# Kernel optimization log

Measured on AMD Instinct MI355X. Metric: run time of the kernel, lower is better.

The kernel has to match this reference:

```python
import jax, jax.numpy as jnp
import numpy as np

V, E, HID, T, B, S = 50000, 256, 512, 9, 64, 512
H = HID // 2
START, STOP = T - 2, T - 1
NEG = -100000.0


def setup_inputs() -> dict:
    key = jax.random.key(0)
    ks = jax.random.split(key, 16)
    sc = 0.05
    tr = jax.random.normal(ks[15], (T, T), jnp.float32)
    tr = tr.at[STOP, :].set(NEG).at[:, START].set(NEG)
    return {
        "batchSentence": jax.random.randint(ks[0], (B, S), 0, V),
        "batchTag": jax.random.randint(ks[1], (B, S), 0, T - 2),
        "lenList": jax.random.randint(ks[2], (B,), 1, S + 1),
        "emb": jax.random.normal(ks[3], (V, E), jnp.float32) * sc,
        "w_ih0": jax.random.normal(ks[4], (2, 4 * H, E), jnp.float32) * sc,
        "w_hh0": jax.random.normal(ks[5], (2, 4 * H, H), jnp.float32) * sc,
        "b_ih0": jax.random.normal(ks[6], (2, 4 * H), jnp.float32) * sc,
        "b_hh0": jax.random.normal(ks[7], (2, 4 * H), jnp.float32) * sc,
        "w_ih1": jax.random.normal(ks[8], (2, 4 * H, 2 * H), jnp.float32) * sc,
        "w_hh1": jax.random.normal(ks[9], (2, 4 * H, H), jnp.float32) * sc,
        "b_ih1": jax.random.normal(ks[10], (2, 4 * H), jnp.float32) * sc,
        "b_hh1": jax.random.normal(ks[11], (2, 4 * H), jnp.float32) * sc,
        "fc_w": jax.random.normal(ks[12], (T, HID), jnp.float32) * sc,
        "fc_b": jax.random.normal(ks[13], (T,), jnp.float32) * sc,
        "transitions": tr,
    }


def _lstm_dir(xs, w_ih, w_hh, b_ih, b_hh, reverse):
    # xs: [S, B, in]; PyTorch gate order i, f, g, o
    h0 = jnp.zeros((xs.shape[1], w_hh.shape[1]), xs.dtype)
    b = b_ih + b_hh

    def step(carry, x_t):
        h, c = carry
        g = x_t @ w_ih.T + h @ w_hh.T + b
        i, f, gg, o = jnp.split(g, 4, axis=-1)
        c = jax.nn.sigmoid(f) * c + jax.nn.sigmoid(i) * jnp.tanh(gg)
        h = jax.nn.sigmoid(o) * jnp.tanh(c)
        return (h, c), h

    _, hs = jax.lax.scan(step, (h0, h0), xs, reverse=reverse)
    return hs


def _bilstm(x, layers):
    xs = x.transpose(1, 0, 2)  # [S, B, E]
    for w_ih, w_hh, b_ih, b_hh in layers:
        fwd = _lstm_dir(xs, w_ih[0], w_hh[0], b_ih[0], b_hh[0], False)
        bwd = _lstm_dir(xs, w_ih[1], w_hh[1], b_ih[1], b_hh[1], True)
        xs = jnp.concatenate([fwd, bwd], axis=-1)
    return xs.transpose(1, 0, 2)  # [B, S, 2H]


def _crf_forward(feats, mask, trans):
    # feats: [B, S, T], mask: [B, S] (t < length)
    start = jnp.full((feats.shape[0], feats.shape[2]), NEG, feats.dtype).at[:, START].set(0.0)

    def step(alpha, inp):
        ft, mt = inp  # [B, T], [B]
        new = jax.nn.logsumexp(alpha[:, :, None] + trans[None, :, :], axis=1) + ft
        return jnp.where(mt[:, None], new, alpha), None

    alpha, _ = jax.lax.scan(step, start, (feats.transpose(1, 0, 2), mask.T))
    return jax.nn.logsumexp(alpha + trans[None, :, STOP], axis=1)


def _gold_score(feats, tags, lengths, trans):
    # Faithful to original _score_sentence, incl. the feats[i][tags[i+1]] indexing
    Ss = feats.shape[1]
    pos = jnp.arange(Ss)
    pair_valid = (pos[None, :-1] + 1) < lengths[:, None]  # step i -> i+1 exists
    em0 = jnp.take_along_axis(feats[:, 0, :], tags[:, :1], axis=1)[:, 0]
    em_shift = jnp.take_along_axis(feats[:, :-1, :], tags[:, 1:, None], axis=2)[:, :, 0]
    tr = trans[tags[:, :-1], tags[:, 1:]]
    body = jnp.sum(jnp.where(pair_valid, tr + em_shift, 0.0), axis=1)
    last_tag = jnp.take_along_axis(tags, (lengths - 1)[:, None], axis=1)[:, 0]
    return trans[START, tags[:, 0]] + em0 + body + trans[last_tag, STOP]


def reference(batchSentence, batchTag, lenList, emb, w_ih0, w_hh0, b_ih0, b_hh0,
              w_ih1, w_hh1, b_ih1, b_hh1, fc_w, fc_b, transitions):
    x = emb[batchSentence]  # [B, S, E]
    h = _bilstm(x, [(w_ih0, w_hh0, b_ih0, b_hh0), (w_ih1, w_hh1, b_ih1, b_hh1)])
    feats = h @ fc_w.T + fc_b  # [B, S, T]
    mask = jnp.arange(feats.shape[1])[None, :] < lenList[:, None]
    forward_score = _crf_forward(feats, mask, transitions)
    gold_score = _gold_score(feats, batchTag, lenList, transitions)
    return jnp.mean(forward_score - gold_score)
```

## Files before the change

### kernel.cpp

```cpp
#include <hip/hip_runtime.h>
#include <math.h>

#define NEGV (-100000.0f)
constexpr int Bn = 64, Sn = 512, En = 256, Hn = 256, HIDn = 512, Tn = 9;
constexpr int START_T = Tn - 2, STOP_T = Tn - 1;
constexpr int Mn = Bn * Sn;

typedef unsigned int u32;
typedef unsigned short u16;
typedef unsigned long long u64;
typedef short short8 __attribute__((ext_vector_type(8)));
typedef float f32x4 __attribute__((ext_vector_type(4)));
typedef int i32x4 __attribute__((ext_vector_type(4)));

__device__ __forceinline__ float sigf(float x) { return 1.0f / (1.0f + __expf(-x)); }
__device__ __forceinline__ float tanh_f(float x) { return 2.0f / (1.0f + __expf(-2.0f * x)) - 1.0f; }
__device__ __forceinline__ u16 f2bf(float f) {
  u32 u = __float_as_uint(f);
  return (u16)((u + 0x7fffu + ((u >> 16) & 1u)) >> 16);
}
__device__ __forceinline__ float bflo(u32 u) { return __uint_as_float(u << 16); }
__device__ __forceinline__ float bfhi(u32 u) { return __uint_as_float(u & 0xffff0000u); }
__device__ __forceinline__ float b2f(u16 v) { return __uint_as_float((u32)v << 16); }

__device__ __forceinline__ void bar_lds() {
  __builtin_amdgcn_sched_barrier(0);
  asm volatile("s_waitcnt lgkmcnt(0)" ::: "memory");
  __builtin_amdgcn_s_barrier();
  __builtin_amdgcn_sched_barrier(0);
}

__global__ void prep_scales(const float* __restrict__ whh0, const float* __restrict__ whh1,
                            float* __restrict__ sw0, float* __restrict__ dqs0,
                            float* __restrict__ sw1, float* __restrict__ dqs1) {
  int r = blockIdx.x * blockDim.x + threadIdx.x;
  if (r >= 2048) return;
  const float* p0 = whh0 + (size_t)r * 256;
  const float* p1 = whh1 + (size_t)r * 256;
  float m0 = 0.f, m1 = 0.f;
  for (int k = 0; k < 256; ++k) {
    m0 = fmaxf(m0, fabsf(p0[k]));
    m1 = fmaxf(m1, fabsf(p1[k]));
  }
  m0 = fmaxf(m0, 1e-8f); m1 = fmaxf(m1, 1e-8f);
  sw0[r] = m0 / 127.f; dqs0[r] = m0 / (127.f * 127.f);
  sw1[r] = m1 / 127.f; dqs1[r] = m1 / (127.f * 127.f);
}

__global__ void prep_kernel(const float* __restrict__ wih0, const float* __restrict__ whh0,
                            const float* __restrict__ bih0, const float* __restrict__ bhh0,
                            const float* __restrict__ wih1, const float* __restrict__ whh1,
                            const float* __restrict__ bih1, const float* __restrict__ bhh1,
                            u16* __restrict__ wifrag0, u16* __restrict__ wifrag1,
                            char* __restrict__ wq0, char* __restrict__ wq1,
                            const float* __restrict__ sw0, const float* __restrict__ sw1,
                            float* __restrict__ bias0, float* __restrict__ bias1) {
  int tid = blockIdx.x * blockDim.x + threadIdx.x;
  int nth = gridDim.x * blockDim.x;
  for (int idx = tid; idx < 524288; idx += nth) {
    int j = idx & 7, lane = (idx >> 3) & 63, ks = (idx >> 9) & 7,
        w2 = (idx >> 12) & 3, nb = (idx >> 14) & 15, d = (idx >> 18) & 1;
    int n = nb * 64 + w2 * 16 + (lane & 15);
    int k = ks * 32 + ((lane >> 4) & 3) * 8 + j;
    wifrag0[idx] = f2bf(wih0[(d * 1024 + n) * 256 + k]);
  }
  for (int idx = tid; idx < 1048576; idx += nth) {
    int j = idx & 7, lane = (idx >> 3) & 63, ks = (idx >> 9) & 15,
        w2 = (idx >> 13) & 3, nb = (idx >> 15) & 15, d = (idx >> 19) & 1;
    int n = nb * 64 + w2 * 16 + (lane & 15);
    int k = ks * 32 + ((lane >> 4) & 3) * 8 + j;
    wifrag1[idx] = f2bf(wih1[(d * 1024 + n) * 512 + k]);
  }
  for (int idx = tid; idx < 524288; idx += nth) {
    int j = idx & 15, lane = (idx >> 4) & 63, kt = (idx >> 10) & 3,
        q = (idx >> 12) & 7, wv = (idx >> 15) & 7, d = (idx >> 18) & 1;
    int nt = q * 8 + wv;
    int n = nt * 16 + (lane & 15);
    int k = kt * 64 + ((lane >> 4) & 3) * 16 + j;
    int row = d * 1024 + n;
    float v0 = whh0[(size_t)row * 256 + k] / sw0[row];
    float v1 = whh1[(size_t)row * 256 + k] / sw1[row];
    wq0[idx] = (char)(int)fminf(fmaxf(rintf(v0), -127.f), 127.f);
    wq1[idx] = (char)(int)fminf(fmaxf(rintf(v1), -127.f), 127.f);
  }
  for (int idx = tid; idx < 2 * 1024; idx += nth) {
    bias0[idx] = bih0[idx] + bhh0[idx];
    bias1[idx] = bih1[idx] + bhh1[idx];
  }
}

template <int KS, bool GATHER>
__global__ __launch_bounds__(256) void gemm_ih(
    const void* __restrict__ xsrc_v,
    const int* __restrict__ sent,
    const uint4* __restrict__ wifrag,
    const float* __restrict__ bias,
    u16* __restrict__ gx2)
{
  constexpr int K = KS * 32;
  constexpr int PITCH = K + 8;
  __shared__ u16 As[64][PITCH];
  const int tid = threadIdx.x;
  const int l = tid & 63;
  const int w = tid >> 6;
  const int col = l & 15;
  const int quad = (l >> 4) & 3;
  const int m0 = blockIdx.x * 64;
  const int dir = blockIdx.y;

  {
    const int lr = tid >> 2, lq = tid & 3;
    if constexpr (GATHER) {
      const float4* xrow = reinterpret_cast<const float4*>(
          (const float*)xsrc_v + (size_t)sent[m0 + lr] * 256) + lq * 16;
      u32* dst = reinterpret_cast<u32*>(&As[lr][lq * 64]);
#pragma unroll
      for (int i = 0; i < 16; ++i) {
        float4 v = xrow[i];
        dst[i * 2 + 0] = (u32)f2bf(v.x) | ((u32)f2bf(v.y) << 16);
        dst[i * 2 + 1] = (u32)f2bf(v.z) | ((u32)f2bf(v.w) << 16);
      }
    } else {
      const uint4* xrow = reinterpret_cast<const uint4*>(
          (const u16*)xsrc_v + (size_t)(m0 + lr) * 512) + lq * 16;
      uint4* dst = reinterpret_cast<uint4*>(&As[lr][lq * 128]);
#pragma unroll
      for (int i = 0; i < 16; ++i) dst[i] = xrow[i];
    }
  }
  __syncthreads();

  const uint4* wfd = wifrag + (size_t)dir * 16 * 4 * KS * 64;
#pragma unroll 1
  for (int nb = 0; nb < 16; ++nb) {
    uint4 bf[KS];
#pragma unroll
    for (int ks = 0; ks < KS; ++ks)
      bf[ks] = wfd[((nb * 4 + w) * KS + ks) * 64 + l];

    f32x4 acc[4];
#pragma unroll
    for (int mt = 0; mt < 4; ++mt) acc[mt] = (f32x4){0.f, 0.f, 0.f, 0.f};
#pragma unroll
    for (int ks = 0; ks < KS; ++ks) {
      short8 b8 = __builtin_bit_cast(short8, bf[ks]);
#pragma unroll
      for (int mt = 0; mt < 4; ++mt) {
        uint4 av = *reinterpret_cast<const uint4*>(&As[mt * 16 + col][ks * 32 + quad * 8]);
        acc[mt] = __builtin_amdgcn_mfma_f32_16x16x32_bf16(
            __builtin_bit_cast(short8, av), b8, acc[mt], 0, 0, 0);
      }
    }

    const int n = nb * 64 + w * 16 + col;
    const int gate = n >> 8, unit = n & 255;
    const float bv = bias[dir * 1024 + n];
#pragma unroll
    for (int mt = 0; mt < 4; ++mt) {
#pragma unroll
      for (int r = 0; r < 4; ++r) {
        int m = m0 + mt * 16 + quad * 4 + r;
        gx2[((size_t)(dir * Mn + m) * 256 + unit) * 4 + gate] = f2bf(acc[mt][r] + bv);
      }
    }
  }
}

__global__ __launch_bounds__(512, 2) void lstm_recur_v12(
    const i32x4* __restrict__ wq,
    const float* __restrict__ dqs,
    const u16* __restrict__ gx2,
    u16* __restrict__ out)
{
  __shared__ char Ah8[2][2][288];
  __shared__ int accW[8][2][32][4];
  const int tid = threadIdx.x;
  const int l = tid & 63;
  const int w = tid >> 6;
  const int col = l & 15;
  const int quad = (l >> 4) & 3;
  const int dir = blockIdx.x >> 5;
  const int bq = blockIdx.x & 31;

  i32x4 bw[8][4];
  {
    const i32x4* wp = wq + ((size_t)dir * 8 + w) * 8 * 4 * 64;
#pragma unroll
    for (int q = 0; q < 8; ++q)
#pragma unroll
      for (int kt = 0; kt < 4; ++kt)
        bw[q][kt] = wp[(q * 4 + kt) * 64 + l];
  }

  const int r_ep = l >> 5;
  const int ue = l & 31;
  const int e_ep = ue >> 4, c_ep = ue & 15;
  const int unit = e_ep * 128 + w * 16 + c_ep;

  float sc[4];
#pragma unroll
  for (int g = 0; g < 4; ++g)
    sc[g] = dqs[dir * 1024 + g * 256 + unit];

  const int mrow = bq * 2 + r_ep;
  const uint2* gp = reinterpret_cast<const uint2*>(gx2) +
                    (size_t)(dir * Mn + mrow * Sn) * 256 + unit;
  u16* op = out + (size_t)mrow * Sn * HIDn + dir * Hn + unit;

  float c_st = 0.f;

  for (int s = 0; s < Sn; ++s) {
    const int t = dir ? (Sn - 1 - s) : s;
    uint2 g2 = gp[(size_t)t * 256];

    if (s > 0) {
      const int rb = (s + 1) & 1;
      i32x4 av[4];
#pragma unroll
      for (int kt = 0; kt < 4; ++kt)
        av[kt] = *reinterpret_cast<const i32x4*>(
            &Ah8[rb][col & 1][kt * 64 + quad * 16]);
      i32x4 acc[8];
#pragma unroll
      for (int q = 0; q < 8; ++q) acc[q] = (i32x4){0, 0, 0, 0};
#pragma unroll
      for (int kt = 0; kt < 4; ++kt)
#pragma unroll
        for (int q = 0; q < 8; ++q)
          acc[q] = __builtin_amdgcn_mfma_i32_16x16x64_i8(av[kt], bw[q][kt], acc[q], 0, 0, 0);
      if (quad == 0) {
#pragma unroll
        for (int e = 0; e < 2; ++e)
#pragma unroll
          for (int r = 0; r < 2; ++r) {
            i32x4 v = (i32x4){acc[0 + e][r], acc[2 + e][r], acc[4 + e][r], acc[6 + e][r]};
            *reinterpret_cast<i32x4*>(&accW[w][r][e * 16 + col][0]) = v;
          }
      }
    }

    float a0 = 0.f, a1 = 0.f, a2 = 0.f, a3 = 0.f;
    if (s > 0) {
      i32x4 q0 = *reinterpret_cast<const i32x4*>(&accW[w][r_ep][ue][0]);
      a0 = (float)q0[0] * sc[0];
      a1 = (float)q0[1] * sc[1];
      a2 = (float)q0[2] * sc[2];
      a3 = (float)q0[3] * sc[3];
    }
    float gi_ = a0 + b2f((u16)(g2.x & 0xffff));
    float gf_ = a1 + b2f((u16)(g2.x >> 16));
    float gg_ = a2 + b2f((u16)(g2.y & 0xffff));
    float go_ = a3 + b2f((u16)(g2.y >> 16));

    c_st = sigf(gf_) * c_st + sigf(gi_) * tanh_f(gg_);
    float h = sigf(go_) * tanh_f(c_st);

    Ah8[s & 1][r_ep][unit] = (char)(int)rintf(h * 127.f);
    op[(size_t)t * HIDn] = f2bf(h);
    bar_lds();
  }
}

__global__ __launch_bounds__(64) void fc_kernel(const u16* __restrict__ out1,
                                                const float* __restrict__ fcw,
                                                const float* __restrict__ fcb,
                                                float* __restrict__ feats) {
  const int bs = blockIdx.x;
  const int l = threadIdx.x;
  const u16* row = out1 + (size_t)bs * HIDn;
  uint4 rv = *reinterpret_cast<const uint4*>(row + l * 8);
  float v[8];
  v[0] = bflo(rv.x); v[1] = bfhi(rv.x);
  v[2] = bflo(rv.y); v[3] = bfhi(rv.y);
  v[4] = bflo(rv.z); v[5] = bfhi(rv.z);
  v[6] = bflo(rv.w); v[7] = bfhi(rv.w);
#pragma unroll
  for (int tag = 0; tag < Tn; ++tag) {
    const float* w = fcw + tag * HIDn + l * 8;
    float4 w0 = *reinterpret_cast<const float4*>(w);
    float4 w1 = *reinterpret_cast<const float4*>(w + 4);
    float acc = v[0] * w0.x + v[1] * w0.y + v[2] * w0.z + v[3] * w0.w
              + v[4] * w1.x + v[5] * w1.y + v[6] * w1.z + v[7] * w1.w;
#pragma unroll
    for (int off = 32; off; off >>= 1) acc += __shfl_xor(acc, off);
    if (l == 0) feats[bs * Tn + tag] = acc + fcb[tag];
  }
}

__global__ __launch_bounds__(64) void crf_kernel(const float* __restrict__ feats,
                                                 const int* __restrict__ tags,
                                                 const int* __restrict__ lens,
                                                 const float* __restrict__ trans,
                                                 float* __restrict__ scores) {
  const int b = blockIdx.x;
  const int j = threadIdx.x;
  const int jj = j < Tn ? j : Tn - 1;
  const int len = lens[b];

  float trc[Tn];
#pragma unroll
  for (int i = 0; i < Tn; ++i) trc[i] = trans[i * Tn + jj];
  const float trS = trans[jj * Tn + STOP_T];

  float alpha = (j == START_T) ? 0.0f : NEGV;
  const float* fb = feats + (size_t)b * Sn * Tn;

  for (int t = 0; t < Sn; ++t) {
    float f = (j < Tn) ? fb[t * Tn + j] : 0.0f;
    float v[Tn];
    float m = -3.0e38f;
#pragma unroll
    for (int i = 0; i < Tn; ++i) {
      float ai = __shfl(alpha, i);
      v[i] = ai + trc[i];
      m = fmaxf(m, v[i]);
    }
    float ssum = 0.0f;
#pragma unroll
    for (int i = 0; i < Tn; ++i) ssum += __expf(v[i] - m);
    float newa = m + __logf(ssum) + f;
    if (t < len && j < Tn) alpha = newa;
  }

  float val = (j < Tn) ? alpha + trS : -3.0e38f;
  float m = val;
#pragma unroll
  for (int off = 32; off; off >>= 1) m = fmaxf(m, __shfl_xor(m, off));
  float se = (j < Tn) ? __expf(val - m) : 0.0f;
#pragma unroll
  for (int off = 32; off; off >>= 1) se += __shfl_xor(se, off);
  float fscore = m + __logf(se);

  const int* tg = tags + b * Sn;
  float part = 0.0f;
  for (int q = 0; q < 8; ++q) {
    int s0 = j * 8 + q;
    if (s0 < Sn - 1 && (s0 + 1) < len) {
      int ta = tg[s0], tb = tg[s0 + 1];
      part += trans[ta * Tn + tb] + fb[s0 * Tn + tb];
    }
  }
#pragma unroll
  for (int off = 32; off; off >>= 1) part += __shfl_xor(part, off);

  if (j == 0) {
    int t0 = tg[0];
    int tl = tg[len - 1];
    float gold = trans[START_T * Tn + t0] + fb[0 * Tn + t0] + part + trans[tl * Tn + STOP_T];
    scores[b] = fscore - gold;
  }
}

__global__ void finalize_kernel(const float* __restrict__ scores, float* __restrict__ out) {
  int l = threadIdx.x;
  float v = scores[l];
#pragma unroll
  for (int off = 32; off; off >>= 1) v += __shfl_xor(v, off);
  if (l == 0) out[0] = v / 64.0f;
}

extern "C" void kernel_launch(void* const* d_in, const int* in_sizes, int n_in,
                              void* d_out, int out_size, void* d_ws, size_t ws_size,
                              hipStream_t stream) {
  const int* sent = (const int*)d_in[0];
  const int* tags = (const int*)d_in[1];
  const int* lens = (const int*)d_in[2];
  const float* emb = (const float*)d_in[3];
  const float* wih0 = (const float*)d_in[4];
  const float* whh0 = (const float*)d_in[5];
  const float* bih0 = (const float*)d_in[6];
  const float* bhh0 = (const float*)d_in[7];
  const float* wih1 = (const float*)d_in[8];
  const float* whh1 = (const float*)d_in[9];
  const float* bih1 = (const float*)d_in[10];
  const float* bhh1 = (const float*)d_in[11];
  const float* fcw = (const float*)d_in[12];
  const float* fcb = (const float*)d_in[13];
  const float* trans = (const float*)d_in[14];

  char* ws = (char*)d_ws;
  u16* outb = (u16*)ws;
  u16* gx2 = (u16*)(ws + 33554432);
  float* feats = (float*)gx2;
  char* p = ws + 33554432 + 134217728;
  float* scores = (float*)p;            p += 256;
  float* bias0 = (float*)p;             p += 8192;
  float* bias1 = (float*)p;             p += 8192;
  u16* wifrag0 = (u16*)p;               p += 1048576;
  u16* wifrag1 = (u16*)p;               p += 2097152;
  char* wq0 = p;                        p += 524288;
  char* wq1 = p;                        p += 524288;
  float* sw0 = (float*)p;               p += 8192;
  float* dqs0 = (float*)p;              p += 8192;
  float* sw1 = (float*)p;               p += 8192;
  float* dqs1 = (float*)p;              p += 8192;

  prep_scales<<<8, 256, 0, stream>>>(whh0, whh1, sw0, dqs0, sw1, dqs1);
  prep_kernel<<<2048, 256, 0, stream>>>(wih0, whh0, bih0, bhh0, wih1, whh1, bih1, bhh1,
                                        wifrag0, wifrag1, wq0, wq1, sw0, sw1, bias0, bias1);

  dim3 ggrid(Mn / 64, 2);
  gemm_ih<8, true><<<ggrid, 256, 0, stream>>>(emb, sent, (const uint4*)wifrag0, bias0, gx2);
  lstm_recur_v12<<<64, 512, 0, stream>>>((const i32x4*)wq0, dqs0, gx2, outb);
  gemm_ih<16, false><<<ggrid, 256, 0, stream>>>(outb, nullptr, (const uint4*)wifrag1, bias1, gx2);
  lstm_recur_v12<<<64, 512, 0, stream>>>((const i32x4*)wq1, dqs1, gx2, outb);

  fc_kernel<<<Mn, 64, 0, stream>>>(outb, fcw, fcb, feats);
  crf_kernel<<<Bn, 64, 0, stream>>>(feats, tags, lens, trans, scores);
  finalize_kernel<<<1, 64, 0, stream>>>(scores, (float*)d_out);
}
```

Before: 1.795 ms.

## Split recurrent MFMA into halves overlapping epilogue; use MFMA for FC layer

The recurrent LSTM step now issues the int8 MFMAs for even accumulator tiles first, publishes them, and runs the gate epilogue for half of the units while the odd-tile MFMAs execute. The other half's epilogue follows. This is meant to hide transcendental and LDS latency in the serial per-step critical path. Separately, the per-row FC projection kernel is replaced with a bf16 MFMA GEMM over 64-row tiles using prearranged weight fragments padded to 16 tags. That reduces launch count and redundant weight loads, at the cost of bf16 rounding of the FC weights.

```diff
diff --git a/kernel.cpp b/kernel.cpp
--- a/kernel.cpp
+++ b/kernel.cpp
@@ -51,10 +51,12 @@
                             const float* __restrict__ bih0, const float* __restrict__ bhh0,
                             const float* __restrict__ wih1, const float* __restrict__ whh1,
                             const float* __restrict__ bih1, const float* __restrict__ bhh1,
+                            const float* __restrict__ fcw,
                             u16* __restrict__ wifrag0, u16* __restrict__ wifrag1,
                             char* __restrict__ wq0, char* __restrict__ wq1,
                             const float* __restrict__ sw0, const float* __restrict__ sw1,
-                            float* __restrict__ bias0, float* __restrict__ bias1) {
+                            float* __restrict__ bias0, float* __restrict__ bias1,
+                            u16* __restrict__ fcfrag) {
   int tid = blockIdx.x * blockDim.x + threadIdx.x;
   int nth = gridDim.x * blockDim.x;
   for (int idx = tid; idx < 524288; idx += nth) {
@@ -82,6 +84,12 @@
     float v1 = whh1[(size_t)row * 256 + k] / sw1[row];
     wq0[idx] = (char)(int)fminf(fmaxf(rintf(v0), -127.f), 127.f);
     wq1[idx] = (char)(int)fminf(fmaxf(rintf(v1), -127.f), 127.f);
+  }
+  for (int idx = tid; idx < 8192; idx += nth) {
+    int j = idx & 7, lane = (idx >> 3) & 63, ks = (idx >> 9) & 15;
+    int tag = lane & 15;
+    int k = ks * 32 + ((lane >> 4) & 3) * 8 + j;
+    fcfrag[idx] = (tag < Tn) ? f2bf(fcw[(size_t)tag * HIDn + k]) : (u16)0;
   }
   for (int idx = tid; idx < 2 * 1024; idx += nth) {
     bias0[idx] = bih0[idx] + bhh0[idx];
@@ -166,7 +174,7 @@
   }
 }
 
-__global__ __launch_bounds__(512, 2) void lstm_recur_v12(
+__global__ __launch_bounds__(512, 2) void lstm_recur_v13(
     const i32x4* __restrict__ wq,
     const float* __restrict__ dqs,
     const u16* __restrict__ gx2,
@@ -213,6 +221,17 @@
     const int t = dir ? (Sn - 1 - s) : s;
     uint2 g2 = gp[(size_t)t * 256];
 
+    auto epi = [&](float a0, float a1, float a2, float a3) {
+      float gi_ = a0 + b2f((u16)(g2.x & 0xffff));
+      float gf_ = a1 + b2f((u16)(g2.x >> 16));
+      float gg_ = a2 + b2f((u16)(g2.y & 0xffff));
+      float go_ = a3 + b2f((u16)(g2.y >> 16));
+      c_st = sigf(gf_) * c_st + sigf(gi_) * tanh_f(gg_);
+      float h = sigf(go_) * tanh_f(c_st);
+      Ah8[s & 1][r_ep][unit] = (char)(int)rintf(h * 127.f);
+      op[(size_t)t * HIDn] = f2bf(h);
+    };
+
     if (s > 0) {
       const int rb = (s + 1) & 1;
       i32x4 av[4];
@@ -220,70 +239,94 @@
       for (int kt = 0; kt < 4; ++kt)
         av[kt] = *reinterpret_cast<const i32x4*>(
             &Ah8[rb][col & 1][kt * 64 + quad * 16]);
+
       i32x4 acc[8];
 #pragma unroll
       for (int q = 0; q < 8; ++q) acc[q] = (i32x4){0, 0, 0, 0};
+
 #pragma unroll
       for (int kt = 0; kt < 4; ++kt)
 #pragma unroll
-        for (int q = 0; q < 8; ++q)
-          acc[q] = __builtin_amdgcn_mfma_i32_16x16x64_i8(av[kt], bw[q][kt], acc[q], 0, 0, 0);
+        for (int g = 0; g < 4; ++g)
+          acc[g * 2] = __builtin_amdgcn_mfma_i32_16x16x64_i8(av[kt], bw[g * 2][kt], acc[g * 2], 0, 0, 0);
       if (quad == 0) {
 #pragma unroll
-        for (int e = 0; e < 2; ++e)
-#pragma unroll
-          for (int r = 0; r < 2; ++r) {
-            i32x4 v = (i32x4){acc[0 + e][r], acc[2 + e][r], acc[4 + e][r], acc[6 + e][r]};
-            *reinterpret_cast<i32x4*>(&accW[w][r][e * 16 + col][0]) = v;
-          }
+        for (int r = 0; r < 2; ++r) {
+          i32x4 v = (i32x4){acc[0][r], acc[2][r], acc[4][r], acc[6][r]};
+          *reinterpret_cast<i32x4*>(&accW[w][r][col][0]) = v;
+        }
       }
-    }
-
-    float a0 = 0.f, a1 = 0.f, a2 = 0.f, a3 = 0.f;
-    if (s > 0) {
-      i32x4 q0 = *reinterpret_cast<const i32x4*>(&accW[w][r_ep][ue][0]);
-      a0 = (float)q0[0] * sc[0];
-      a1 = (float)q0[1] * sc[1];
-      a2 = (float)q0[2] * sc[2];
-      a3 = (float)q0[3] * sc[3];
-    }
-    float gi_ = a0 + b2f((u16)(g2.x & 0xffff));
-    float gf_ = a1 + b2f((u16)(g2.x >> 16));
-    float gg_ = a2 + b2f((u16)(g2.y & 0xffff));
-    float go_ = a3 + b2f((u16)(g2.y >> 16));
-
-    c_st = sigf(gf_) * c_st + sigf(gi_) * tanh_f(gg_);
-    float h = sigf(go_) * tanh_f(c_st);
-
-    Ah8[s & 1][r_ep][unit] = (char)(int)rintf(h * 127.f);
-    op[(size_t)t * HIDn] = f2bf(h);
+      i32x4 qA = *reinterpret_cast<const i32x4*>(&accW[w][r_ep][ue][0]);
+
+#pragma unroll
+      for (int kt = 0; kt < 4; ++kt)
+#pragma unroll
+        for (int g = 0; g < 4; ++g)
+          acc[g * 2 + 1] = __builtin_amdgcn_mfma_i32_16x16x64_i8(av[kt], bw[g * 2 + 1][kt], acc[g * 2 + 1], 0, 0, 0);
+
+      if (ue < 16)
+        epi((float)qA[0] * sc[0], (float)qA[1] * sc[1],
+            (float)qA[2] * sc[2], (float)qA[3] * sc[3]);
+
+      if (quad == 0) {
+#pragma unroll
+        for (int r = 0; r < 2; ++r) {
+          i32x4 v = (i32x4){acc[1][r], acc[3][r], acc[5][r], acc[7][r]};
+          *reinterpret_cast<i32x4*>(&accW[w][r][16 + col][0]) = v;
+        }
+      }
+      i32x4 qB = *reinterpret_cast<const i32x4*>(&accW[w][r_ep][ue][0]);
+      if (ue >= 16)
+        epi((float)qB[0] * sc[0], (float)qB[1] * sc[1],
+            (float)qB[2] * sc[2], (float)qB[3] * sc[3]);
+    } else {
+      epi(0.f, 0.f, 0.f, 0.f);
+    }
     bar_lds();
   }
 }
 
-__global__ __launch_bounds__(64) void fc_kernel(const u16* __restrict__ out1,
-                                                const float* __restrict__ fcw,
-                                                const float* __restrict__ fcb,
-                                                float* __restrict__ feats) {
-  const int bs = blockIdx.x;
-  const int l = threadIdx.x;
-  const u16* row = out1 + (size_t)bs * HIDn;
-  uint4 rv = *reinterpret_cast<const uint4*>(row + l * 8);
-  float v[8];
-  v[0] = bflo(rv.x); v[1] = bfhi(rv.x);
-  v[2] = bflo(rv.y); v[3] = bfhi(rv.y);
-  v[4] = bflo(rv.z); v[5] = bfhi(rv.z);
-  v[6] = bflo(rv.w); v[7] = bfhi(rv.w);
-#pragma unroll
-  for (int tag = 0; tag < Tn; ++tag) {
-    const float* w = fcw + tag * HIDn + l * 8;
-    float4 w0 = *reinterpret_cast<const float4*>(w);
-    float4 w1 = *reinterpret_cast<const float4*>(w + 4);
-    float acc = v[0] * w0.x + v[1] * w0.y + v[2] * w0.z + v[3] * w0.w
-              + v[4] * w1.x + v[5] * w1.y + v[6] * w1.z + v[7] * w1.w;
-#pragma unroll
-    for (int off = 32; off; off >>= 1) acc += __shfl_xor(acc, off);
-    if (l == 0) feats[bs * Tn + tag] = acc + fcb[tag];
+__global__ __launch_bounds__(256) void fc_mfma(const u16* __restrict__ out1,
+                                               const uint4* __restrict__ fcfrag,
+                                               const float* __restrict__ fcb,
+                                               float* __restrict__ feats) {
+  __shared__ u16 As[64][520];
+  const int tid = threadIdx.x;
+  const int l = tid & 63;
+  const int w = tid >> 6;
+  const int col = l & 15;
+  const int quad = (l >> 4) & 3;
+  const int m0 = blockIdx.x * 64;
+
+  {
+    const int lr = tid >> 2, lq = tid & 3;
+    const uint4* xrow = reinterpret_cast<const uint4*>(
+        out1 + (size_t)(m0 + lr) * 512) + lq * 16;
+    uint4* dst = reinterpret_cast<uint4*>(&As[lr][lq * 128]);
+#pragma unroll
+    for (int i = 0; i < 16; ++i) dst[i] = xrow[i];
+  }
+  __syncthreads();
+
+  uint4 bf[16];
+#pragma unroll
+  for (int ks = 0; ks < 16; ++ks) bf[ks] = fcfrag[ks * 64 + l];
+
+  f32x4 acc = (f32x4){0.f, 0.f, 0.f, 0.f};
+#pragma unroll
+  for (int ks = 0; ks < 16; ++ks) {
+    uint4 av = *reinterpret_cast<const uint4*>(&As[w * 16 + col][ks * 32 + quad * 8]);
+    acc = __builtin_amdgcn_mfma_f32_16x16x32_bf16(
+        __builtin_bit_cast(short8, av), __builtin_bit_cast(short8, bf[ks]), acc, 0, 0, 0);
+  }
+
+  if (col < Tn) {
+    const float bv = fcb[col];
+#pragma unroll
+    for (int r = 0; r < 4; ++r) {
+      int m = m0 + w * 16 + quad * 4 + r;
+      feats[(size_t)m * Tn + col] = acc[r] + bv;
+    }
   }
 }
 
@@ -394,18 +437,20 @@
   float* dqs0 = (float*)p;              p += 8192;
   float* sw1 = (float*)p;               p += 8192;
   float* dqs1 = (float*)p;              p += 8192;
+  u16* fcfrag = (u16*)p;                p += 16384;
 
   prep_scales<<<8, 256, 0, stream>>>(whh0, whh1, sw0, dqs0, sw1, dqs1);
-  prep_kernel<<<2048, 256, 0, stream>>>(wih0, whh0, bih0, bhh0, wih1, whh1, bih1, bhh1,
-                                        wifrag0, wifrag1, wq0, wq1, sw0, sw1, bias0, bias1);
+  prep_kernel<<<2048, 256, 0, stream>>>(wih0, whh0, bih0, bhh0, wih1, whh1, bih1, bhh1, fcw,
+                                        wifrag0, wifrag1, wq0, wq1, sw0, sw1, bias0, bias1,
+                                        fcfrag);
 
   dim3 ggrid(Mn / 64, 2);
   gemm_ih<8, true><<<ggrid, 256, 0, stream>>>(emb, sent, (const uint4*)wifrag0, bias0, gx2);
-  lstm_recur_v12<<<64, 512, 0, stream>>>((const i32x4*)wq0, dqs0, gx2, outb);
+  lstm_recur_v13<<<64, 512, 0, stream>>>((const i32x4*)wq0, dqs0, gx2, outb);
   gemm_ih<16, false><<<ggrid, 256, 0, stream>>>(outb, nullptr, (const uint4*)wifrag1, bias1, gx2);
-  lstm_recur_v12<<<64, 512, 0, stream>>>((const i32x4*)wq1, dqs1, gx2, outb);
-
-  fc_kernel<<<Mn, 64, 0, stream>>>(outb, fcw, fcb, feats);
+  lstm_recur_v13<<<64, 512, 0, stream>>>((const i32x4*)wq1, dqs1, gx2, outb);
+
+  fc_mfma<<<Mn / 64, 256, 0, stream>>>(outb, (const uint4*)fcfrag, fcb, feats);
   crf_kernel<<<Bn, 64, 0, stream>>>(feats, tags, lens, trans, scores);
   finalize_kernel<<<1, 64, 0, stream>>>(scores, (float*)d_out);
 }
```

Result: slower. 2.070 ms (+15.3%).
